# Optimization experiments

Hardware: AMD Instinct MI355X
Metric: run time of the kernel (lower is better)

## Reference

```python
import jax, jax.numpy as jnp
import numpy as np
import math

D_MODEL = 1024; NHEAD = 16; HEAD_DIM = D_MODEL // NHEAD
MOE_HIDDEN = 2048; NUM_EXPERTS = 4; TOP_K = 2
DECOMP_KS = (7, 25, 49)
B = 8; N = 1024
LN_EPS = 1e-5

def _alibi_slopes(n):
    start = 2.0 ** (-2.0 ** (-(math.log2(n) - 3)))
    return np.array([start * (start ** i) for i in range(n)], dtype=np.float32)

ALIBI = jnp.asarray(_alibi_slopes(NHEAD))  # [H]

def setup_inputs() -> dict:
    key = jax.random.key(0)
    ks = jax.random.split(key, 16)
    rn = lambda k, s, sc=0.02: jax.random.normal(k, s, dtype=jnp.float32) * sc
    z = lambda s: jnp.zeros(s, jnp.float32)
    inp = {}
    inp['x'] = jax.random.normal(ks[0], (B, N, D_MODEL), dtype=jnp.float32)
    inp['qw'] = rn(ks[1], (D_MODEL, D_MODEL)); inp['qb'] = z((D_MODEL,))
    inp['kw'] = rn(ks[2], (D_MODEL, D_MODEL)); inp['kb'] = z((D_MODEL,))
    inp['vw'] = rn(ks[3], (D_MODEL, D_MODEL)); inp['vb'] = z((D_MODEL,))
    inp['ow'] = rn(ks[4], (D_MODEL, D_MODEL)); inp['ob'] = z((D_MODEL,))
    inp['n1g'] = jnp.ones((D_MODEL,), jnp.float32); inp['n1b'] = z((D_MODEL,))
    inp['n2g'] = jnp.ones((D_MODEL,), jnp.float32); inp['n2b'] = z((D_MODEL,))
    inp['alpha'] = z((len(DECOMP_KS),))
    # depthwise moving-average kernels (module inits to 1/k); add jitter so grads are non-trivial
    inp['dw7'] = jnp.full((D_MODEL, 1, 7), 1.0 / 7, jnp.float32) + rn(ks[5], (D_MODEL, 1, 7), 0.01)
    inp['dw25'] = jnp.full((D_MODEL, 1, 25), 1.0 / 25, jnp.float32) + rn(ks[6], (D_MODEL, 1, 25), 0.01)
    inp['dw49'] = jnp.full((D_MODEL, 1, 49), 1.0 / 49, jnp.float32) + rn(ks[7], (D_MODEL, 1, 49), 0.01)
    inp['router_w'] = rn(ks[8], (NUM_EXPERTS, D_MODEL))
    inp['ew1'] = rn(ks[9], (NUM_EXPERTS, MOE_HIDDEN, D_MODEL)); inp['eb1'] = z((NUM_EXPERTS, MOE_HIDDEN))
    inp['ew2'] = rn(ks[10], (NUM_EXPERTS, D_MODEL, MOE_HIDDEN)); inp['eb2'] = z((NUM_EXPERTS, D_MODEL))
    inp['tw'] = rn(ks[11], (D_MODEL, 1, 5)); inp['tb'] = z((D_MODEL,))
    return inp

def _ln(x, g, b):
    m = jnp.mean(x, axis=-1, keepdims=True)
    v = jnp.mean((x - m) ** 2, axis=-1, keepdims=True)
    return (x - m) * jax.lax.rsqrt(v + LN_EPS) * g + b

def _dwconv(x_bdn, w):  # depthwise 1D conv, VALID padding; w: [D,1,k]
    return jax.lax.conv_general_dilated(
        x_bdn, w, window_strides=(1,), padding='VALID',
        feature_group_count=D_MODEL, dimension_numbers=('NCH', 'OIH', 'NCH'))

def _forward(x, qw, qb, kw, kb, vw, vb, ow, ob, n1g, n1b, n2g, n2b,
             alpha, dw7, dw25, dw49, router_w, ew1, eb1, ew2, eb2, tw, tb):
    # ---- Decomp1D: multi-kernel depthwise moving averages, softmax-mixed ----
    xt = jnp.transpose(x, (0, 2, 1))  # [B, D, N]
    trends = []
    for w_, k in zip((dw7, dw25, dw49), DECOMP_KS):
        xp = jnp.pad(xt, ((0, 0), (0, 0), (k // 2, k // 2)), mode='reflect')
        trends.append(_dwconv(xp, w_))  # [B, D, N]
    wts = jax.nn.softmax(alpha)
    Tr = sum(wi * ti for wi, ti in zip(wts, trends))  # trend [B, D, N]
    Tr = jnp.transpose(Tr, (0, 2, 1))  # [B, N, D]
    S = x - Tr                          # seasonal
    # ---- ALiBi self-attention on normalized seasonal part ----
    Sn = _ln(S, n1g, n1b)
    split = lambda h: jnp.transpose(h.reshape(B, N, NHEAD, HEAD_DIM), (0, 2, 1, 3))
    q = split(Sn @ qw.T + qb)
    k = split(Sn @ kw.T + kb)
    v = split(Sn @ vw.T + vb)
    logits = jnp.einsum('bhqd,bhkd->bhqk', q, k) / math.sqrt(HEAD_DIM)
    idx = jnp.arange(N)
    dist = jnp.clip(idx[None, :] - idx[:, None], 0, None).astype(jnp.float32)  # (j-i)+
    logits = logits - ALIBI[None, :, None, None] * dist[None, None]
    attn = jax.nn.softmax(logits, axis=-1)
    y = jnp.einsum('bhqk,bhkd->bhqd', attn, v)
    y = jnp.transpose(y, (0, 2, 1, 3)).reshape(B, N, D_MODEL) @ ow.T + ob
    x_s = S + y
    # ---- top-2 gated MoE FFN (no capacity limit) ----
    xf = _ln(x_s, n2g, n2b).reshape(B * N, D_MODEL)
    gates = jax.nn.softmax(xf @ router_w.T, axis=-1)  # [T, E]
    topv, topi = jax.lax.top_k(gates, TOP_K)
    topv = topv / jnp.clip(jnp.sum(topv, axis=-1, keepdims=True), 1e-9, None)
    weights = jnp.zeros_like(gates).at[jnp.arange(B * N)[:, None], topi].set(topv)
    aux = NUM_EXPERTS * jnp.sum(jnp.mean(gates, axis=0) *
                                jnp.mean((weights > 0).astype(jnp.float32), axis=0))
    out = jnp.zeros_like(xf)
    for e in range(NUM_EXPERTS):  # small fixed expert count
        h = jax.nn.gelu(xf @ ew1[e].T + eb1[e], approximate=False)
        out = out + (h @ ew2[e].T + eb2[e]) * weights[:, e:e + 1]
    x_s = x_s + out.reshape(B, N, D_MODEL)
    # ---- trend depthwise conv (k=5, zero padding=2, bias) ----
    tp = jnp.pad(jnp.transpose(Tr, (0, 2, 1)), ((0, 0), (0, 0), (2, 2)))
    t_out = _dwconv(tp, tw) + tb[None, :, None]
    return (x_s + jnp.transpose(t_out, (0, 2, 1)), aux)

def reference(x, qw, qb, kw, kb, vw, vb, ow, ob, n1g, n1b, n2g, n2b,
              alpha, dw7, dw25, dw49, router_w, ew1, eb1, ew2, eb2, tw, tb):
    return _forward(x, qw, qb, kw, kb, vw, vb, ow, ob, n1g, n1b, n2g, n2b,
                    alpha, dw7, dw25, dw49, router_w, ew1, eb1, ew2, eb2, tw, tb)
```

## Files before the change

kernel.cpp:

```cpp
#include <hip/hip_runtime.h>
#include <hip/hip_bf16.h>
#include <math.h>

using bf16 = __hip_bfloat16;
typedef __attribute__((ext_vector_type(8))) short s8v;
typedef __attribute__((ext_vector_type(4))) float f32x4;

#define D_MODEL 1024
#define NB 8
#define SEQ 1024
#define NHEAD 16
#define HD 64
#define MOE_H 2048
#define TOKENS (NB*SEQ)
#define QKV_S 3072

__global__ void f2b_k(const float* __restrict__ in, bf16* __restrict__ out, int n) {
    int i = blockIdx.x * blockDim.x + threadIdx.x;
    int stride = gridDim.x * blockDim.x;
    for (; i < n; i += stride) out[i] = __float2bfloat16(in[i]);
}

__global__ void cat3_k(const float* __restrict__ a, const float* __restrict__ b,
                       const float* __restrict__ c, float* __restrict__ o) {
    int i = blockIdx.x * blockDim.x + threadIdx.x;
    if (i < 1024) o[i] = a[i];
    else if (i < 2048) o[i] = b[i - 1024];
    else if (i < 3072) o[i] = c[i - 2048];
}

__global__ void prefix_k(const int* __restrict__ cnt, int* __restrict__ off) {
    if (threadIdx.x == 0 && blockIdx.x == 0) {
        int s = 0;
        for (int e = 0; e < 4; e++) { off[e] = s; s += cnt[e]; }
    }
}

#define TN 128
#define TD 64
__global__ __launch_bounds__(256) void decomp_k(
    const float* __restrict__ x, const float* __restrict__ alpha,
    const float* __restrict__ dw7, const float* __restrict__ dw25,
    const float* __restrict__ dw49, float* __restrict__ Tr, float* __restrict__ S)
{
    __shared__ float xs[TN + 48][TD];
    const int n0 = blockIdx.x * TN, d0 = blockIdx.y * TD, b = blockIdx.z;
    for (int i = threadIdx.x; i < (TN + 48) * (TD / 4); i += 256) {
        int r = i / (TD / 4), c4 = (i % (TD / 4)) * 4;
        int n = n0 + r - 24;
        if (n < 0) n = -n;
        if (n > SEQ - 1) n = 2 * (SEQ - 1) - n;
        *(float4*)&xs[r][c4] =
            *(const float4*)&x[((size_t)(b * SEQ + n)) * D_MODEL + d0 + c4];
    }
    float a0 = alpha[0], a1 = alpha[1], a2 = alpha[2];
    float mx = fmaxf(a0, fmaxf(a1, a2));
    float e0 = __expf(a0 - mx), e1 = __expf(a1 - mx), e2 = __expf(a2 - mx);
    float inv = 1.0f / (e0 + e1 + e2);
    float w7 = e0 * inv, w25 = e1 * inv, w49 = e2 * inv;
    const int dl = threadIdx.x & 63;
    const int nt = threadIdx.x >> 6;
    const int d = d0 + dl;
    float w[49];
    #pragma unroll
    for (int j = 0; j < 49; j++) {
        float v = w49 * dw49[d * 49 + j];
        if (j >= 12 && j < 37) v += w25 * dw25[d * 25 + j - 12];
        if (j >= 21 && j < 28) v += w7 * dw7[d * 7 + j - 21];
        w[j] = v;
    }
    __syncthreads();
    for (int nl = nt; nl < TN; nl += 4) {
        float acc = 0.f;
        #pragma unroll
        for (int j = 0; j < 49; j++) acc = fmaf(xs[nl + j][dl], w[j], acc);
        size_t idx = ((size_t)(b * SEQ + n0 + nl)) * D_MODEL + d;
        Tr[idx] = acc;
        S[idx] = xs[nl + 24][dl] - acc;
    }
}

__global__ __launch_bounds__(256) void ln_k(
    const float* __restrict__ x, const float* __restrict__ g, const float* __restrict__ b,
    bf16* __restrict__ ob, float* __restrict__ of)
{
    int row = blockIdx.x, t = threadIdx.x;
    const float* xr = x + (size_t)row * D_MODEL;
    float s = 0.f, s2 = 0.f;
    for (int d = t; d < D_MODEL; d += 256) { float v = xr[d]; s += v; s2 += v * v; }
    #pragma unroll
    for (int o = 32; o > 0; o >>= 1) { s += __shfl_down(s, o); s2 += __shfl_down(s2, o); }
    __shared__ float sh[8];
    int wid = t >> 6, lane = t & 63;
    if (lane == 0) { sh[wid] = s; sh[4 + wid] = s2; }
    __syncthreads();
    if (t == 0) {
        float ts = sh[0] + sh[1] + sh[2] + sh[3];
        float t2 = sh[4] + sh[5] + sh[6] + sh[7];
        float m = ts / D_MODEL;
        float var = t2 / D_MODEL - m * m;
        sh[0] = m; sh[1] = rsqrtf(var + 1e-5f);
    }
    __syncthreads();
    float m = sh[0], rs = sh[1];
    for (int d = t; d < D_MODEL; d += 256) {
        float v = (xr[d] - m) * rs * g[d] + b[d];
        ob[(size_t)row * D_MODEL + d] = __float2bfloat16(v);
        if (of) of[(size_t)row * D_MODEL + d] = v;
    }
}

template<int ACT, int OMODE, int GMODE>
__global__ __launch_bounds__(512, 4) void gemm_nt(
    const bf16* __restrict__ A, const bf16* __restrict__ B,
    const float* __restrict__ bias, const float* resid,
    const float* __restrict__ rowscale, int rs_stride,
    void* C, int M, int K, int O,
    const int* __restrict__ row_map, const int* __restrict__ cnt_ptr,
    const int* __restrict__ off_ptr, size_t b_estride, int bias_estride)
{
    const int bm = blockIdx.x, bn = blockIdx.y;
    const int e = (GMODE != 0) ? blockIdx.z : 0;
    int M_act = M;
    int off = 0;
    const int* rmap = row_map;
    if (GMODE != 0) {
        M_act = cnt_ptr[e];
        if (bm * 128 >= M_act) return;
        off = off_ptr[e];
        rmap = row_map + e * TOKENS;
        B += (size_t)e * b_estride;
        if (bias) bias += (size_t)e * bias_estride;
    }
    __shared__ bf16 As[128][72];
    __shared__ bf16 Bs[128][72];
    const int t = threadIdx.x;
    const int lane = t & 63, wid = t >> 6;
    const int wm = wid >> 1, wn = wid & 1;
    f32x4 acc[2][4] = {};
    const int lr = t >> 3;
    const int lc = (t & 7) * 8;
    const size_t abase = (GMODE == 2) ? (size_t)(off + bm * 128) * K : (size_t)(bm * 128) * K;
    const size_t bbase = (size_t)(bn * 128) * K;
    size_t arow[2];
    #pragma unroll
    for (int p = 0; p < 2; p++) {
        int r = p * 64 + lr;
        if (GMODE == 1) {
            int gr = bm * 128 + r;
            arow[p] = (size_t)rmap[gr < M_act ? gr : M_act - 1] * K;
        } else {
            arow[p] = abase + (size_t)r * K;
        }
    }
    s8v ra[2], rb[2];
    #pragma unroll
    for (int p = 0; p < 2; p++) {
        ra[p] = *(const s8v*)&A[arow[p] + lc];
        rb[p] = *(const s8v*)&B[bbase + (size_t)(p * 64 + lr) * K + lc];
    }
    for (int k0 = 0; k0 < K; k0 += 64) {
        #pragma unroll
        for (int p = 0; p < 2; p++) {
            int r = p * 64 + lr;
            *(s8v*)&As[r][lc] = ra[p];
            *(s8v*)&Bs[r][lc] = rb[p];
        }
        __syncthreads();
        if (k0 + 64 < K) {
            const int kn = k0 + 64 + lc;
            #pragma unroll
            for (int p = 0; p < 2; p++) {
                ra[p] = *(const s8v*)&A[arow[p] + kn];
                rb[p] = *(const s8v*)&B[bbase + (size_t)(p * 64 + lr) * K + kn];
            }
        }
        const int fr = lane & 15, fq = (lane >> 4) * 8;
        #pragma unroll
        for (int kk = 0; kk < 64; kk += 32) {
            s8v af[2], bfr[4];
            #pragma unroll
            for (int i = 0; i < 2; i++)
                af[i] = *(const s8v*)&As[wm * 32 + i * 16 + fr][kk + fq];
            #pragma unroll
            for (int j = 0; j < 4; j++)
                bfr[j] = *(const s8v*)&Bs[wn * 64 + j * 16 + fr][kk + fq];
            #pragma unroll
            for (int i = 0; i < 2; i++)
                #pragma unroll
                for (int j = 0; j < 4; j++)
                    acc[i][j] = __builtin_amdgcn_mfma_f32_16x16x32_bf16(af[i], bfr[j], acc[i][j], 0, 0, 0);
        }
        __syncthreads();
    }
    const int cr = lane & 15, quad = lane >> 4;
    #pragma unroll
    for (int i = 0; i < 2; i++) {
        #pragma unroll
        for (int r = 0; r < 4; r++) {
            int row = bm * 128 + wm * 32 + i * 16 + quad * 4 + r;
            if (GMODE != 0 && row >= M_act) continue;
            int srow = (GMODE == 2) ? rmap[row] : ((GMODE == 1) ? off + row : row);
            #pragma unroll
            for (int j = 0; j < 4; j++) {
                int col = bn * 128 + wn * 64 + j * 16 + cr;
                float v = acc[i][j][r];
                if (bias) v += bias[col];
                if (ACT == 1) v = 0.5f * v * (1.0f + erff(v * 0.70710678118f));
                size_t idx = (size_t)srow * O + col;
                if (OMODE == 0) {
                    float rv = resid ? resid[idx] : 0.0f;
                    ((float*)C)[idx] = rv + v;
                } else if (OMODE == 1) {
                    ((bf16*)C)[idx] = __float2bfloat16(v);
                } else {
                    atomicAdd(&((float*)C)[idx], rowscale[(size_t)srow * rs_stride + e] * v);
                }
            }
        }
    }
}

__global__ __launch_bounds__(256) void attn_k(
    const bf16* __restrict__ QKV, bf16* __restrict__ Y)
{
    __shared__ bf16 Ks[64][72];
    __shared__ bf16 Vt[64][66];
    __shared__ bf16 Pw[4][32][72];
    const int t = threadIdx.x;
    const int wave = t >> 6, lane = t & 63;
    const int qm = lane & 15, quad = lane >> 4;
    const int b = blockIdx.z, h = blockIdx.y;
    const int qbase = blockIdx.x * 128 + wave * 32;
    const float LOG2E = 1.44269504f;
    const float slope2 = exp2f(-0.5f * (float)(h + 1)) * LOG2E;
    const float NEG8L2 = -11.54156036f;
    const float SCL2   = 0.18033688f;

    s8v qa[2][2];
    #pragma unroll
    for (int g = 0; g < 2; g++) {
        const bf16* qp = QKV + ((size_t)(b * SEQ + qbase + g * 16 + qm)) * QKV_S + h * HD;
        qa[g][0] = *(const s8v*)&qp[quad * 8];
        qa[g][1] = *(const s8v*)&qp[32 + quad * 8];
    }
    float aqp[2][4];
    #pragma unroll
    for (int g = 0; g < 2; g++)
        #pragma unroll
        for (int r = 0; r < 4; r++)
            aqp[g][r] = slope2 * (float)(qbase + g * 16 + quad * 4 + r) + NEG8L2;

    f32x4 o[2][4] = {};
    float l[2][4] = {};

    const int sr = t >> 2;
    const int scc = (t & 3) * 16;
    const bf16* kvb = QKV + (size_t)(b * SEQ) * QKV_S + D_MODEL + h * HD + scc;

    {
        const bf16* p0 = kvb + (size_t)sr * QKV_S;
        s8v k0v = *(const s8v*)&p0[0];
        s8v k1v = *(const s8v*)&p0[8];
        s8v v0  = *(const s8v*)&p0[D_MODEL];
        s8v v1  = *(const s8v*)&p0[D_MODEL + 8];

        for (int k0 = 0; k0 < SEQ; k0 += 64) {
            *(s8v*)&Ks[sr][scc] = k0v;
            *(s8v*)&Ks[sr][scc + 8] = k1v;
            #pragma unroll
            for (int j = 0; j < 8; j++) {
                Vt[scc + j][sr]     = ((const bf16*)&v0)[j];
                Vt[scc + 8 + j][sr] = ((const bf16*)&v1)[j];
            }
            __syncthreads();
            if (k0 + 64 < SEQ) {
                const bf16* np = kvb + (size_t)(k0 + 64 + sr) * QKV_S;
                k0v = *(const s8v*)&np[0];
                k1v = *(const s8v*)&np[8];
                v0  = *(const s8v*)&np[D_MODEL];
                v1  = *(const s8v*)&np[D_MODEL + 8];
            }
            float bk[4];
            #pragma unroll
            for (int jt = 0; jt < 4; jt++) bk[jt] = slope2 * (float)(k0 + jt * 16 + qm);
            #pragma unroll
            for (int g = 0; g < 2; g++) {
                f32x4 scr[4];
                #pragma unroll
                for (int jt = 0; jt < 4; jt++) {
                    f32x4 z = {};
                    s8v b0 = *(const s8v*)&Ks[jt * 16 + qm][quad * 8];
                    s8v b1 = *(const s8v*)&Ks[jt * 16 + qm][32 + quad * 8];
                    z = __builtin_amdgcn_mfma_f32_16x16x32_bf16(qa[g][0], b0, z, 0, 0, 0);
                    z = __builtin_amdgcn_mfma_f32_16x16x32_bf16(qa[g][1], b1, z, 0, 0, 0);
                    scr[jt] = z;
                }
                #pragma unroll
                for (int jt = 0; jt < 4; jt++) {
                    #pragma unroll
                    for (int r = 0; r < 4; r++) {
                        float term = fminf(aqp[g][r] - bk[jt], NEG8L2);
                        float pf = exp2f(fmaf(scr[jt][r], SCL2, term));
                        bf16 pb = __float2bfloat16(pf);
                        l[g][r] += __bfloat162float(pb);
                        Pw[wave][g * 16 + quad * 4 + r][jt * 16 + qm] = pb;
                    }
                }
            }
            __builtin_amdgcn_wave_barrier();
            #pragma unroll
            for (int g = 0; g < 2; g++) {
                s8v pa0 = *(const s8v*)&Pw[wave][g * 16 + qm][quad * 8];
                s8v pa1 = *(const s8v*)&Pw[wave][g * 16 + qm][32 + quad * 8];
                #pragma unroll
                for (int dt = 0; dt < 4; dt++) {
                    s8v vb0 = *(const s8v*)&Vt[dt * 16 + qm][quad * 8];
                    s8v vb1 = *(const s8v*)&Vt[dt * 16 + qm][32 + quad * 8];
                    o[g][dt] = __builtin_amdgcn_mfma_f32_16x16x32_bf16(pa0, vb0, o[g][dt], 0, 0, 0);
                    o[g][dt] = __builtin_amdgcn_mfma_f32_16x16x32_bf16(pa1, vb1, o[g][dt], 0, 0, 0);
                }
            }
            __syncthreads();
        }
    }
    #pragma unroll
    for (int g = 0; g < 2; g++)
        #pragma unroll
        for (int r = 0; r < 4; r++) {
            float s = l[g][r];
            s += __shfl_xor(s, 1); s += __shfl_xor(s, 2);
            s += __shfl_xor(s, 4); s += __shfl_xor(s, 8);
            l[g][r] = 1.0f / s;
        }
    #pragma unroll
    for (int g = 0; g < 2; g++)
        #pragma unroll
        for (int dt = 0; dt < 4; dt++)
            #pragma unroll
            for (int r = 0; r < 4; r++) {
                size_t idx = ((size_t)(b * SEQ + qbase + g * 16 + quad * 4 + r)) * D_MODEL + h * HD + dt * 16 + qm;
                Y[idx] = __float2bfloat16(o[g][dt][r] * l[g][r]);
            }
}

__global__ __launch_bounds__(256) void router_k(
    const float* __restrict__ xf, const float* __restrict__ rw,
    float* __restrict__ wts, float* __restrict__ auxb,
    int* __restrict__ cnt, int* __restrict__ elist)
{
    const int wave = threadIdx.x >> 6, lane = threadIdx.x & 63;
    float4 w[4][4];
    #pragma unroll
    for (int e = 0; e < 4; e++)
        #pragma unroll
        for (int c = 0; c < 4; c++)
            w[e][c] = *(const float4*)&rw[e * D_MODEL + lane * 16 + c * 4];
    float ag[4] = {0.f, 0.f, 0.f, 0.f};
    float ac[4] = {0.f, 0.f, 0.f, 0.f};
    __shared__ int sel[16][2];
    __shared__ float sh[4][8];
    const int t0 = (blockIdx.x * 4 + wave) * 4;
    #pragma unroll
    for (int i = 0; i < 4; i++) {
        const int tk = t0 + i;
        const float* xr = xf + (size_t)tk * D_MODEL + lane * 16;
        float4 xv[4];
        #pragma unroll
        for (int c = 0; c < 4; c++) xv[c] = *(const float4*)&xr[c * 4];
        float p[4] = {0.f, 0.f, 0.f, 0.f};
        #pragma unroll
        for (int e = 0; e < 4; e++)
            #pragma unroll
            for (int c = 0; c < 4; c++) {
                p[e] = fmaf(xv[c].x, w[e][c].x, p[e]);
                p[e] = fmaf(xv[c].y, w[e][c].y, p[e]);
                p[e] = fmaf(xv[c].z, w[e][c].z, p[e]);
                p[e] = fmaf(xv[c].w, w[e][c].w, p[e]);
            }
        #pragma unroll
        for (int o = 1; o < 64; o <<= 1) {
            p[0] += __shfl_xor(p[0], o); p[1] += __shfl_xor(p[1], o);
            p[2] += __shfl_xor(p[2], o); p[3] += __shfl_xor(p[3], o);
        }
        float g[4];
        float mx = fmaxf(fmaxf(p[0], p[1]), fmaxf(p[2], p[3]));
        float se = 0.f;
        #pragma unroll
        for (int e = 0; e < 4; e++) { g[e] = __expf(p[e] - mx); se += g[e]; }
        #pragma unroll
        for (int e = 0; e < 4; e++) g[e] /= se;
        int i1 = 0; float v1 = g[0];
        #pragma unroll
        for (int e = 1; e < 4; e++) if (g[e] > v1) { v1 = g[e]; i1 = e; }
        int i2 = -1; float v2 = -1.f;
        #pragma unroll
        for (int e = 0; e < 4; e++) if (e != i1 && g[e] > v2) { v2 = g[e]; i2 = e; }
        float sw = fmaxf(v1 + v2, 1e-9f);
        if (lane < 4) {
            float wv = (lane == i1) ? v1 / sw : ((lane == i2) ? v2 / sw : 0.f);
            wts[(size_t)tk * 4 + lane] = wv;
        }
        if (lane == 0) {
            #pragma unroll
            for (int e = 0; e < 4; e++) ag[e] += g[e];
            ac[i1] += 1.f; ac[i2] += 1.f;
            sel[wave * 4 + i][0] = i1;
            sel[wave * 4 + i][1] = i2;
        }
    }
    if (lane == 0)
        #pragma unroll
        for (int e = 0; e < 4; e++) { sh[wave][e] = ag[e]; sh[wave][4 + e] = ac[e]; }
    __syncthreads();
    if (threadIdx.x < 8) {
        float s = sh[0][threadIdx.x] + sh[1][threadIdx.x] + sh[2][threadIdx.x] + sh[3][threadIdx.x];
        atomicAdd(&auxb[threadIdx.x], s);
    }
    if (threadIdx.x < 4) {
        const int e = threadIdx.x;
        int loc[16]; int c = 0;
        #pragma unroll
        for (int s = 0; s < 16; s++)
            if (sel[s][0] == e || sel[s][1] == e) loc[c++] = blockIdx.x * 16 + s;
        if (c) {
            int base = atomicAdd(&cnt[e], c);
            for (int k = 0; k < c; k++) elist[e * TOKENS + base + k] = loc[k];
        }
    }
}

__global__ __launch_bounds__(256) void final_k(
    const float* __restrict__ xs, const float* __restrict__ Tr,
    const float* __restrict__ tw, const float* __restrict__ tb, float* __restrict__ out)
{
    int n = blockIdx.x, b = blockIdx.y, t = threadIdx.x;
    for (int d = t; d < D_MODEL; d += 256) {
        float acc = tb[d];
        #pragma unroll
        for (int j = 0; j < 5; j++) {
            int i = n + j - 2;
            if (i >= 0 && i < SEQ)
                acc += Tr[((size_t)(b * SEQ + i)) * D_MODEL + d] * tw[d * 5 + j];
        }
        size_t idx = ((size_t)(b * SEQ + n)) * D_MODEL + d;
        out[idx] = xs[idx] + acc;
    }
}

__global__ void aux_k(const float* __restrict__ ab, float* __restrict__ out) {
    if (threadIdx.x == 0 && blockIdx.x == 0) {
        float a = 0.f;
        for (int e = 0; e < 4; e++)
            a += (ab[e] / (float)TOKENS) * (ab[4 + e] / (float)TOKENS);
        out[0] = 4.0f * a;
    }
}

extern "C" void kernel_launch(void* const* d_in, const int* in_sizes, int n_in,
                              void* d_out, int out_size, void* d_ws, size_t ws_size,
                              hipStream_t stream)
{
    const float* x    = (const float*)d_in[0];
    const float* qw   = (const float*)d_in[1];
    const float* qb   = (const float*)d_in[2];
    const float* kw   = (const float*)d_in[3];
    const float* kb   = (const float*)d_in[4];
    const float* vw   = (const float*)d_in[5];
    const float* vb   = (const float*)d_in[6];
    const float* ow   = (const float*)d_in[7];
    const float* ob   = (const float*)d_in[8];
    const float* n1g  = (const float*)d_in[9];
    const float* n1b  = (const float*)d_in[10];
    const float* n2g  = (const float*)d_in[11];
    const float* n2b  = (const float*)d_in[12];
    const float* alpha= (const float*)d_in[13];
    const float* dw7  = (const float*)d_in[14];
    const float* dw25 = (const float*)d_in[15];
    const float* dw49 = (const float*)d_in[16];
    const float* rw   = (const float*)d_in[17];
    const float* ew1  = (const float*)d_in[18];
    const float* eb1  = (const float*)d_in[19];
    const float* ew2  = (const float*)d_in[20];
    const float* eb2  = (const float*)d_in[21];
    const float* tw   = (const float*)d_in[22];
    const float* tb   = (const float*)d_in[23];

    char* ws = (char*)d_ws;
    const size_t MBy = 1ull << 20;
    float* S    = (float*)(ws + 0 * MBy);
    float* Tr   = (float*)(ws + 32 * MBy);
    float* XF   = (float*)(ws + 64 * MBy);
    bf16*  SNB  = (bf16*)(ws + 96 * MBy);
    bf16*  QKVB = (bf16*)(ws + 112 * MBy);
    bf16*  XFB  = (bf16*)(ws + 160 * MBy);
    bf16*  WQ   = (bf16*)(ws + 176 * MBy);
    bf16*  WK   = (bf16*)(ws + 178 * MBy);
    bf16*  WV   = (bf16*)(ws + 180 * MBy);
    bf16*  WO   = (bf16*)(ws + 182 * MBy);
    bf16*  WE1  = (bf16*)(ws + 184 * MBy);
    bf16*  WE2  = (bf16*)(ws + 200 * MBy);
    float* WTS  = (float*)(ws + 216 * MBy);
    float* AUXB = (float*)(ws + 217 * MBy);
    int*   CNT  = (int*)(AUXB + 8);
    int*   OFF  = CNT + 4;
    float* QKVBIAS = (float*)(ws + 217 * MBy + 4096);
    int*   ELST = (int*)(ws + 218 * MBy);
    bf16*  YB = SNB;
    bf16*  HALL = (bf16*)(ws + 96 * MBy);

    f2b_k<<<2048, 256, 0, stream>>>(qw, WQ, D_MODEL * D_MODEL);
    f2b_k<<<2048, 256, 0, stream>>>(kw, WK, D_MODEL * D_MODEL);
    f2b_k<<<2048, 256, 0, stream>>>(vw, WV, D_MODEL * D_MODEL);
    f2b_k<<<2048, 256, 0, stream>>>(ow, WO, D_MODEL * D_MODEL);
    f2b_k<<<4096, 256, 0, stream>>>(ew1, WE1, 4 * MOE_H * D_MODEL);
    f2b_k<<<4096, 256, 0, stream>>>(ew2, WE2, 4 * D_MODEL * MOE_H);
    cat3_k<<<12, 256, 0, stream>>>(qb, kb, vb, QKVBIAS);

    decomp_k<<<dim3(SEQ / TN, D_MODEL / TD, NB), 256, 0, stream>>>(x, alpha, dw7, dw25, dw49, Tr, S);

    ln_k<<<TOKENS, 256, 0, stream>>>(S, n1g, n1b, SNB, nullptr);

    gemm_nt<0, 1, 0><<<dim3(64, 24), 512, 0, stream>>>(SNB, WQ, QKVBIAS, nullptr, nullptr, 0, QKVB, TOKENS, D_MODEL, QKV_S, nullptr, nullptr, nullptr, 0, 0);

    attn_k<<<dim3(SEQ / 128, NHEAD, NB), 256, 0, stream>>>(QKVB, YB);

    gemm_nt<0, 0, 0><<<dim3(64, 8), 512, 0, stream>>>(YB, WO, ob, S, nullptr, 0, S, TOKENS, D_MODEL, D_MODEL, nullptr, nullptr, nullptr, 0, 0);

    ln_k<<<TOKENS, 256, 0, stream>>>(S, n2g, n2b, XFB, XF);

    hipMemsetAsync(AUXB, 0, 64, stream);
    router_k<<<TOKENS / 16, 256, 0, stream>>>(XF, rw, WTS, AUXB, CNT, ELST);
    prefix_k<<<1, 64, 0, stream>>>(CNT, OFF);

    gemm_nt<1, 1, 1><<<dim3(64, MOE_H / 128, 4), 512, 0, stream>>>(
        XFB, WE1, eb1, nullptr, nullptr, 0, HALL, TOKENS, D_MODEL, MOE_H,
        ELST, CNT, OFF, (size_t)MOE_H * D_MODEL, MOE_H);
    gemm_nt<0, 2, 2><<<dim3(64, D_MODEL / 128, 4), 512, 0, stream>>>(
        HALL, WE2, eb2, nullptr, WTS, 4, S, TOKENS, MOE_H, D_MODEL,
        ELST, CNT, OFF, (size_t)D_MODEL * MOE_H, D_MODEL);

    final_k<<<dim3(SEQ, NB), 256, 0, stream>>>(S, Tr, tw, tb, (float*)d_out);
    aux_k<<<1, 64, 0, stream>>>(AUXB, (float*)d_out + (out_size - 1));
}
```

Baseline: 889.5 us.

## Double-buffer GEMM LDS tiles with two-deep register prefetch

Rewrites the bf16 MFMA GEMM main loop to ping-pong between two LDS buffers, keeping two K-tiles of global loads in flight in registers. It uses one barrier per tile instead of two, with an explicit lgkmcnt wait plus a sched_barrier, so global loads and LDS writes overlap with MFMA compute. The cost is double the LDS footprint (about 72KB per block), which may reduce occupancy. The loop also assumes K/64 is even and at least 3.

```diff
diff --git a/kernel.cpp b/kernel.cpp
--- a/kernel.cpp
+++ b/kernel.cpp
@@ -132,8 +132,8 @@
         B += (size_t)e * b_estride;
         if (bias) bias += (size_t)e * bias_estride;
     }
-    __shared__ bf16 As[128][72];
-    __shared__ bf16 Bs[128][72];
+    __shared__ bf16 As[2][128][72];
+    __shared__ bf16 Bs[2][128][72];
     const int t = threadIdx.x;
     const int lane = t & 63, wid = t >> 6;
     const int wm = wid >> 1, wn = wid & 1;
@@ -153,46 +153,55 @@
             arow[p] = abase + (size_t)r * K;
         }
     }
-    s8v ra[2], rb[2];
-    #pragma unroll
-    for (int p = 0; p < 2; p++) {
-        ra[p] = *(const s8v*)&A[arow[p] + lc];
-        rb[p] = *(const s8v*)&B[bbase + (size_t)(p * 64 + lr) * K + lc];
-    }
-    for (int k0 = 0; k0 < K; k0 += 64) {
-        #pragma unroll
-        for (int p = 0; p < 2; p++) {
-            int r = p * 64 + lr;
-            *(s8v*)&As[r][lc] = ra[p];
-            *(s8v*)&Bs[r][lc] = rb[p];
-        }
-        __syncthreads();
-        if (k0 + 64 < K) {
-            const int kn = k0 + 64 + lc;
-            #pragma unroll
-            for (int p = 0; p < 2; p++) {
-                ra[p] = *(const s8v*)&A[arow[p] + kn];
-                rb[p] = *(const s8v*)&B[bbase + (size_t)(p * 64 + lr) * K + kn];
-            }
-        }
-        const int fr = lane & 15, fq = (lane >> 4) * 8;
-        #pragma unroll
-        for (int kk = 0; kk < 64; kk += 32) {
-            s8v af[2], bfr[4];
-            #pragma unroll
-            for (int i = 0; i < 2; i++)
-                af[i] = *(const s8v*)&As[wm * 32 + i * 16 + fr][kk + fq];
-            #pragma unroll
-            for (int j = 0; j < 4; j++)
-                bfr[j] = *(const s8v*)&Bs[wn * 64 + j * 16 + fr][kk + fq];
-            #pragma unroll
-            for (int i = 0; i < 2; i++)
-                #pragma unroll
-                for (int j = 0; j < 4; j++)
-                    acc[i][j] = __builtin_amdgcn_mfma_f32_16x16x32_bf16(af[i], bfr[j], acc[i][j], 0, 0, 0);
-        }
-        __syncthreads();
-    }
+    const int nt = K / 64;
+
+#define LOADT(RA, RB, TT) do { const int kn_ = (TT) * 64 + lc;                      \
+    _Pragma("unroll") for (int p_ = 0; p_ < 2; p_++) {                              \
+        RA[p_] = *(const s8v*)&A[arow[p_] + kn_];                                   \
+        RB[p_] = *(const s8v*)&B[bbase + (size_t)(p_ * 64 + lr) * K + kn_]; } } while (0)
+#define WRITET(BUF, RA, RB) do {                                                    \
+    _Pragma("unroll") for (int p_ = 0; p_ < 2; p_++) {                              \
+        *(s8v*)&As[BUF][p_ * 64 + lr][lc] = RA[p_];                                 \
+        *(s8v*)&Bs[BUF][p_ * 64 + lr][lc] = RB[p_]; } } while (0)
+#define LBAR() do { asm volatile("s_waitcnt lgkmcnt(0)" ::: "memory");              \
+    __builtin_amdgcn_sched_barrier(0); __builtin_amdgcn_s_barrier(); } while (0)
+#define COMPUTE(BUF) do {                                                           \
+    _Pragma("unroll") for (int kk_ = 0; kk_ < 64; kk_ += 32) {                      \
+        s8v af_[2], bf_[4];                                                         \
+        _Pragma("unroll") for (int i_ = 0; i_ < 2; i_++)                            \
+            af_[i_] = *(const s8v*)&As[BUF][wm * 32 + i_ * 16 + fr][kk_ + fq];      \
+        _Pragma("unroll") for (int j_ = 0; j_ < 4; j_++)                            \
+            bf_[j_] = *(const s8v*)&Bs[BUF][wn * 64 + j_ * 16 + fr][kk_ + fq];      \
+        _Pragma("unroll") for (int i_ = 0; i_ < 2; i_++)                            \
+            _Pragma("unroll") for (int j_ = 0; j_ < 4; j_++)                        \
+                acc[i_][j_] = __builtin_amdgcn_mfma_f32_16x16x32_bf16(af_[i_], bf_[j_], acc[i_][j_], 0, 0, 0); \
+    } } while (0)
+
+    const int fr = lane & 15, fq = (lane >> 4) * 8;
+    s8v r0a[2], r0b[2], r1a[2], r1b[2];
+    LOADT(r0a, r0b, 0);
+    WRITET(0, r0a, r0b);
+    LOADT(r1a, r1b, 1);
+    LOADT(r0a, r0b, 2);
+    LBAR();
+
+    for (int tt = 0; tt < nt; tt += 2) {
+        WRITET(1, r1a, r1b);
+        if (tt + 3 < nt) LOADT(r1a, r1b, tt + 3);
+        COMPUTE(0);
+        LBAR();
+        if (tt + 2 < nt) {
+            WRITET(0, r0a, r0b);
+            if (tt + 4 < nt) LOADT(r0a, r0b, tt + 4);
+        }
+        COMPUTE(1);
+        LBAR();
+    }
+#undef LOADT
+#undef WRITET
+#undef LBAR
+#undef COMPUTE
+
     const int cr = lane & 15, quad = lane >> 4;
     #pragma unroll
     for (int i = 0; i < 2; i++) {
```

New measurement: 858.5 us. 3.5% less time.
